# Kernel tuning notes

Hardware: AMD Instinct MI355X
Metric: run time of the kernel (lower is better)

## Reference

```python
import jax, jax.numpy as jnp
import numpy as np

EPS = 1e-5  # nn.BatchNorm2d default eps


def _cbs(x, w, g, b, m, v):
    # Conv(k=1, bias=False) + BatchNorm2d(inference) + SiLU
    y = jnp.einsum('bchw,oc->bohw', x, w)
    s = (g * jax.lax.rsqrt(v + EPS))[None, :, None, None]
    y = (y - m[None, :, None, None]) * s + b[None, :, None, None]
    return y * jax.nn.sigmoid(y)


def setup_inputs():
    key = jax.random.key(0)
    B, D, H, W = 1, 256, 80, 80
    C = D // 2
    ks = jax.random.split(key, 20)
    r = lambda i, shape, sc=1.0: jax.random.normal(ks[i], shape, dtype=jnp.float32) * sc
    oC, oD = jnp.ones((C,), jnp.float32), jnp.ones((D,), jnp.float32)
    zC, zD = jnp.zeros((C,), jnp.float32), jnp.zeros((D,), jnp.float32)
    return {
        'x': r(0, (B, D, H, W)),
        'w1': r(1, (C, D), 0.05), 'g1': oC, 'b1': zC, 'm1': zC, 'v1': oC,
        'w2': r(2, (D, C), 0.05), 'g2': oD, 'b2': zD, 'm2': zD, 'v2': oD,
        'w3': r(3, (D, C), 0.05), 'g3': oD, 'b3': zD, 'm3': zD, 'v3': oD,
        'wq': r(4, (C, C), 0.05), 'bq': r(5, (C,), 0.01),
        'wk': r(6, (C, C), 0.05), 'bk': r(7, (C,), 0.01),
        'wv': r(8, (C, C), 0.05), 'bv': r(9, (C,), 0.01),
        'wp': r(10, (C, C), 0.05), 'bp': r(11, (C,), 0.01),
        'rel_h': r(12, (1, C, H, 1)), 'rel_w': r(13, (1, C, 1, W)),
        'ef_h': r(14, (1, C, H, 1)), 'ef_w': r(15, (1, C, 1, W)),
    }


def reference(x, w1, g1, b1, m1, v1, w2, g2, b2, m2, v2, w3, g3, b3, m3, v3,
              wq, bq, wk, bk, wv, bv, wp, bp, rel_h, rel_w, ef_h, ef_w):
    x1 = _cbs(x, w1, g1, b1, m1, v1)            # [B, C, H, W]
    B, C, H, W = x1.shape
    HW = H * W
    proj = lambda w, b: (jnp.einsum('bchw,oc->bohw', x1, w)
                         + b[None, :, None, None]).reshape(B, C, HW)
    q = proj(wq, bq)
    k = proj(wk, bk)
    v = proj(wv, bv)
    p = proj(wp, bp)
    # content-content + content-position attention branch
    cp = (rel_h + rel_w).reshape(C, HW)          # [C, HW]
    cc = jnp.einsum('bci,bcj->bij', q, k)        # [B, HW, HW]
    cpos = jnp.einsum('ci,bcj->bij', cp, q)      # [B, HW, HW]
    attn = jax.nn.softmax(cc + cpos, axis=-1)
    # out1[b,c,i] = sum_j v[b,c,j] * attn[b,i,j]  (bmm(v, attn^T))
    out1 = jnp.einsum('bcj,bij->bci', v, attn).reshape(B, C, H, W)
    # extra positional branch (valid because B == 1)
    ef = (ef_h + ef_w).reshape(B, C, HW)         # [1, C, HW]
    ce = jnp.einsum('bci,bcj->bij', p, ef)       # [B, HW, HW]
    eng = jax.nn.softmax(ce, axis=-1)
    out2 = jnp.einsum('bcj,bij->bci', ef, eng).reshape(B, C, H, W)
    return x + _cbs(out1, w2, g2, b2, m2, v2) + _cbs(out2, w3, g3, b3, m3, v3)
```

## Files before the change

kernel.cpp:

```cpp
#include <hip/hip_runtime.h>


typedef unsigned short u16;
typedef __attribute__((ext_vector_type(8))) short bf16x8;
typedef __attribute__((ext_vector_type(4))) float f32x4;
typedef __attribute__((ext_vector_type(4))) unsigned int u32x4;

#define HW 6400
#define BN_EPS 1e-5f

__device__ __forceinline__ u16 f2b(float f) {
  unsigned u = __float_as_uint(f);
  u += 0x7fffu + ((u >> 16) & 1u);
  return (u16)(u >> 16);
}
__device__ __forceinline__ unsigned pack2(float a, float b) {
  return (unsigned)f2b(a) | ((unsigned)f2b(b) << 16);
}
__device__ __forceinline__ f32x4 MFMA(bf16x8 a, bf16x8 b, f32x4 c) {
  return __builtin_amdgcn_mfma_f32_16x16x32_bf16(a, b, c, 0, 0, 0);
}
__device__ __forceinline__ float silu_f(float y) {
  return y / (1.0f + __expf(-y));
}
__device__ __forceinline__ bf16x8 pack8(f32x4 lo, f32x4 hi, float sc) {
  union { bf16x8 v; uint4 u; } r;
  r.u.x = pack2(lo[0] * sc, lo[1] * sc);
  r.u.y = pack2(lo[2] * sc, lo[3] * sc);
  r.u.z = pack2(hi[0] * sc, hi[1] * sc);
  r.u.w = pack2(hi[2] * sc, hi[3] * sc);
  return r.v;
}
__device__ __forceinline__ void unpack8(bf16x8 v, f32x4& lo, f32x4& hi) {
  union { bf16x8 v; unsigned short e[8]; } u; u.v = v;
#pragma unroll
  for (int k = 0; k < 4; ++k) {
    lo[k] = __uint_as_float((unsigned)u.e[k] << 16);
    hi[k] = __uint_as_float((unsigned)u.e[k + 4] << 16);
  }
}
__device__ __forceinline__ void gload_lds16(const u16* src, u16* dst) {
  __builtin_amdgcn_global_load_lds(
      (const __attribute__((address_space(1))) void*)src,
      (__attribute__((address_space(3))) void*)dst, 16, 0, 0);
}

__global__ void prep_all(
    const float* __restrict__ rel_h, const float* __restrict__ rel_w,
    const float* __restrict__ ef_h, const float* __restrict__ ef_w,
    const float* __restrict__ w1, const float* __restrict__ g1, const float* __restrict__ b1,
    const float* __restrict__ m1, const float* __restrict__ v1,
    const float* __restrict__ w2, const float* __restrict__ g2, const float* __restrict__ b2,
    const float* __restrict__ m2, const float* __restrict__ v2,
    const float* __restrict__ w3, const float* __restrict__ g3, const float* __restrict__ b3,
    const float* __restrict__ m3, const float* __restrict__ v3,
    const float* __restrict__ wq, const float* __restrict__ bq,
    const float* __restrict__ wk, const float* __restrict__ bk,
    const float* __restrict__ wv, const float* __restrict__ bv,
    const float* __restrict__ wp, const float* __restrict__ bp,
    u16* __restrict__ LT,
    u16* __restrict__ w1b, float* __restrict__ b1e,
    u16* __restrict__ Wcat, float* __restrict__ bcat,
    u16* __restrict__ w2b, float* __restrict__ b2e,
    u16* __restrict__ w3b, float* __restrict__ b3e,
    u16* __restrict__ efhT, u16* __restrict__ efwT,
    u16* __restrict__ efhB, u16* __restrict__ efwB,
    float* __restrict__ lbuf)
{
  const int b = blockIdx.x;
  const int t = threadIdx.x;
  if (b < 80) {
    const int h = b;
    const int c0 = (t & 63) * 2;
    const float rh0 = rel_h[c0 * 80 + h], rh1 = rel_h[(c0 + 1) * 80 + h];
    for (int wcol = (t >> 6); wcol < 80; wcol += 4) {
      const int i = h * 80 + wcol;
      float rw0 = rel_w[c0 * 80 + wcol], rw1 = rel_w[(c0 + 1) * 80 + wcol];
      *(unsigned*)&LT[(size_t)i * 256 + 128 + c0] = pack2(rh0 + rw0, rh1 + rw1);
    }
  } else if (b < 144) {
    const int tid = (b - 80) * 256 + t;
    const int stride = 64 * 256;
    for (int idx = tid; idx < 128 * 256; idx += stride) {
      int o = idx >> 8;
      float s = g1[o] * rsqrtf(v1[o] + BN_EPS);
      w1b[idx] = f2b(w1[idx] * s);
    }
    for (int idx = tid; idx < 128; idx += stride) {
      float s = g1[idx] * rsqrtf(v1[idx] + BN_EPS);
      b1e[idx] = b1[idx] - m1[idx] * s;
    }
    for (int idx = tid; idx < 4 * 128 * 128; idx += stride) {
      int which = idx >> 14, r = idx & 16383;
      const float* src = which == 0 ? wq : which == 1 ? wk : which == 2 ? wv : wp;
      Wcat[idx] = f2b(src[r]);
    }
    for (int idx = tid; idx < 512; idx += stride) {
      int which = idx >> 7, r = idx & 127;
      const float* src = which == 0 ? bq : which == 1 ? bk : which == 2 ? bv : bp;
      bcat[idx] = src[r];
    }
    for (int idx = tid; idx < 256 * 128; idx += stride) {
      int o = idx >> 7;
      float s2 = g2[o] * rsqrtf(v2[o] + BN_EPS);
      w2b[idx] = f2b(w2[idx] * s2);
      float s3 = g3[o] * rsqrtf(v3[o] + BN_EPS);
      w3b[idx] = f2b(w3[idx] * s3);
    }
    for (int idx = tid; idx < 256; idx += stride) {
      float s2 = g2[idx] * rsqrtf(v2[idx] + BN_EPS);
      b2e[idx] = b2[idx] - m2[idx] * s2;
      float s3 = g3[idx] * rsqrtf(v3[idx] + BN_EPS);
      b3e[idx] = b3[idx] - m3[idx] * s3;
    }
    for (int idx = tid; idx < 80 * 128; idx += stride) {
      int hj = idx >> 7, c = idx & 127;
      efhT[idx] = f2b(ef_h[c * 80 + hj]);
      efwT[idx] = f2b(ef_w[c * 80 + hj]);
    }
    for (int idx = tid; idx < 128 * 96; idx += stride) {
      int c = idx / 96, hj = idx % 96;
      efhB[idx] = hj < 80 ? f2b(ef_h[c * 80 + hj]) : (u16)0;
      efwB[idx] = hj < 80 ? f2b(ef_w[c * 80 + hj]) : (u16)0;
    }
  } else {
    const int tid = (b - 144) * 256 + t;
    const int stride = 32 * 256;
    for (int idx = tid; idx < HW / 4; idx += stride)
      ((f32x4*)lbuf)[idx] = (f32x4){0.f, 0.f, 0.f, 0.f};
  }
}

__global__ __launch_bounds__(256) void front_k(
    const float* __restrict__ x,
    const u16* __restrict__ w1b, const float* __restrict__ b1e,
    const u16* __restrict__ Wcat, const float* __restrict__ bcat,
    u16* __restrict__ LT, u16* __restrict__ RT, u16* __restrict__ Vv,
    u16* __restrict__ pT)
{
  __shared__ __align__(16) float xs[16][260];
  __shared__ __align__(16) u16 tr[16][136];
  const int t = threadIdx.x, lane = t & 63, w = t >> 6, jl = lane & 15, q = lane >> 4;
  const bool partA = blockIdx.x < 400;
  const int ib = partA ? blockIdx.x : blockIdx.x - 400;
  const int i0 = ib * 16;

#pragma unroll
  for (int pp = 0; pp < 4; ++pp) {
    const int p = w * 4 + pp;
    const int ch = p * 16 + (lane >> 2);
    const int ii = (lane & 3) * 4;
    f32x4 v = *(const f32x4*)(x + (size_t)ch * HW + i0 + ii);
    xs[ii][ch] = v[0]; xs[ii + 1][ch] = v[1];
    xs[ii + 2][ch] = v[2]; xs[ii + 3][ch] = v[3];
  }
  __syncthreads();

  bf16x8 afr[8];
#pragma unroll
  for (int ks = 0; ks < 8; ++ks) {
    f32x4 va = *(const f32x4*)&xs[jl][ks * 32 + q * 8];
    f32x4 vb = *(const f32x4*)&xs[jl][ks * 32 + q * 8 + 4];
    afr[ks] = pack8(va, vb, 1.0f);
  }
  f32x4 acc[2];
#pragma unroll
  for (int nn = 0; nn < 2; ++nn) acc[nn] = (f32x4){0.f, 0.f, 0.f, 0.f};
#pragma unroll
  for (int ks = 0; ks < 8; ++ks)
#pragma unroll
    for (int nn = 0; nn < 2; ++nn) {
      const int nf = w * 2 + nn;
      bf16x8 b = *(const bf16x8*)(w1b + (size_t)(nf * 16 + jl) * 256 + ks * 32 + q * 8);
      acc[nn] = MFMA(afr[ks], b, acc[nn]);
    }
#pragma unroll
  for (int nn = 0; nn < 2; ++nn) {
    const int c = (w * 2 + nn) * 16 + jl;
    const float bias = b1e[c];
#pragma unroll
    for (int r = 0; r < 4; ++r)
      tr[q * 4 + r][c] = f2b(silu_f(acc[nn][r] + bias));
  }
  __syncthreads();
  bf16x8 xa[4];
#pragma unroll
  for (int ks = 0; ks < 4; ++ks)
    xa[ks] = *(const bf16x8*)&tr[jl][ks * 32 + q * 8];

  for (int ncl = 0; ncl < 2; ++ncl) {
    const int nc = (partA ? 0 : 2) + ncl;
    f32x4 a2[2];
#pragma unroll
    for (int nn = 0; nn < 2; ++nn) a2[nn] = (f32x4){0.f, 0.f, 0.f, 0.f};
#pragma unroll
    for (int ks = 0; ks < 4; ++ks)
#pragma unroll
      for (int nn = 0; nn < 2; ++nn) {
        const int nf = w * 2 + nn;
        bf16x8 b = *(const bf16x8*)(Wcat + (size_t)(nc * 128 + nf * 16 + jl) * 128 + ks * 32 + q * 8);
        a2[nn] = MFMA(xa[ks], b, a2[nn]);
      }
    if (nc == 2) {
#pragma unroll
      for (int nn = 0; nn < 2; ++nn) {
        const int c = (w * 2 + nn) * 16 + jl;
        const float bias = bcat[256 + c];
        uint2 pk;
        pk.x = pack2(a2[nn][0] + bias, a2[nn][1] + bias);
        pk.y = pack2(a2[nn][2] + bias, a2[nn][3] + bias);
        *(uint2*)(Vv + (size_t)c * HW + i0 + q * 4) = pk;
      }
    } else {
      __syncthreads();
#pragma unroll
      for (int nn = 0; nn < 2; ++nn) {
        const int c = (w * 2 + nn) * 16 + jl;
        const float bias = bcat[nc * 128 + c];
#pragma unroll
        for (int r = 0; r < 4; ++r)
          tr[q * 4 + r][c] = f2b(a2[nn][r] + bias);
      }
      __syncthreads();
#pragma unroll
      for (int rr = 0; rr < 4; ++rr) {
        const int r = w * 4 + rr;
        unsigned val = *(const unsigned*)&tr[r][lane * 2];
        const size_t row = (size_t)(i0 + r);
        if (nc == 0) {
          *(unsigned*)(LT + row * 256 + lane * 2) = val;
          *(unsigned*)(RT + row * 256 + 128 + lane * 2) = val;
        } else if (nc == 1) {
          *(unsigned*)(RT + row * 256 + lane * 2) = val;
        } else {
          *(unsigned*)(pT + row * 128 + lane * 2) = val;
        }
      }
    }
  }
}

__global__ __launch_bounds__(512, 2) void fused_attn(
    const u16* __restrict__ LT,
    const u16* __restrict__ RT,
    const u16* __restrict__ Vv,
    u16* __restrict__ Opart,
    float* __restrict__ lv)
{
  __shared__ __align__(1024) u16 Rs[2][128 * 128];
  __shared__ __align__(1024) u16 Ts[2][64 * 128];
  const int t = threadIdx.x, lane = t & 63, w = t >> 6, jl = lane & 15, q = lane >> 4;
  const int bid = blockIdx.x;
  const int jp = bid / 50, it = bid % 50;
  const int wi = w & 1, wj = w >> 1;
  const int i0w = it * 128 + wi * 64;
  u16* Tw = Ts[wi];

  bf16x8 afr[4][8];
#pragma unroll
  for (int mt = 0; mt < 4; ++mt)
#pragma unroll
    for (int l = 0; l < 8; ++l)
      afr[mt][l] = *(const bf16x8*)(LT + (size_t)(i0w + mt * 16 + jl) * 256 + l * 32 + q * 8);

  f32x4 o[4][2];
#pragma unroll
  for (int mt = 0; mt < 4; ++mt)
#pragma unroll
    for (int cf = 0; cf < 2; ++cf) o[mt][cf] = (f32x4){0.f, 0.f, 0.f, 0.f};
  float lacc[4] = {0.f, 0.f, 0.f, 0.f};

  auto stage_half = [&](int jj, int b) {
#pragma unroll
    for (int cl = 0; cl < 4; ++cl) {
      const int cc = w * 4 + cl;
      const int jr = cc * 4 + (lane >> 4);
      const int cp = lane & 15;
      const int ch = (cp & ~7) | ((cp ^ jr) & 7);
      gload_lds16(RT + (size_t)(jj + jr) * 256 + b * 128 + ch * 8,
                  Rs[b] + (cc << 9));
    }
  };

  stage_half(jp * 1280, 0);
  stage_half(jp * 1280, 1);

  for (int stp = 0; stp < 10; ++stp) {
    const int jj = jp * 1280 + stp * 128;

    f32x4 s[2][4];
#pragma unroll
    for (int nf = 0; nf < 2; ++nf)
#pragma unroll
      for (int mt = 0; mt < 4; ++mt) s[nf][mt] = (f32x4){0.f, 0.f, 0.f, 0.f};

    __syncthreads();

#pragma unroll
    for (int h = 0; h < 2; ++h)
#pragma unroll
      for (int nf = 0; nf < 2; ++nf) {
        const int row = wj * 32 + nf * 16 + jl;
#pragma unroll
        for (int l = 0; l < 4; ++l) {
          const int ch = (l * 4 + q) ^ (jl & 7);
          bf16x8 b = *(const bf16x8*)(Rs[h] + row * 128 + ch * 8);
          s[nf][0] = MFMA(b, afr[0][h * 4 + l], s[nf][0]);
          s[nf][1] = MFMA(b, afr[1][h * 4 + l], s[nf][1]);
          s[nf][2] = MFMA(b, afr[2][h * 4 + l], s[nf][2]);
          s[nf][3] = MFMA(b, afr[3][h * 4 + l], s[nf][3]);
        }
      }
    __syncthreads();
    if (stp < 9) stage_half(jj + 128, 0);

#pragma unroll
    for (int nf = 0; nf < 2; ++nf)
#pragma unroll
      for (int mt = 0; mt < 4; ++mt)
#pragma unroll
        for (int r = 0; r < 4; ++r) {
          float p = __expf(s[nf][mt][r]);
          s[nf][mt][r] = p;
          lacc[mt] += p;
        }

#pragma unroll
    for (int mt = 0; mt < 4; ++mt)
#pragma unroll
      for (int nf = 0; nf < 2; ++nf) {
        const int row = mt * 16 + jl;
        const int cs = (wj * 8 + nf * 4 + q) ^ ((jl & 7) << 2);
        uint2 pk;
        pk.x = pack2(s[nf][mt][0], s[nf][mt][1]);
        pk.y = pack2(s[nf][mt][2], s[nf][mt][3]);
        *(uint2*)(Tw + row * 128 + cs * 4) = pk;
      }
    __syncthreads();
    if (stp < 9) stage_half(jj + 128, 1);

#pragma unroll
    for (int ks2 = 0; ks2 < 4; ++ks2) {
      bf16x8 bv0 = *(const bf16x8*)(Vv + (size_t)(wj * 32 + jl) * HW + jj + ks2 * 32 + q * 8);
      bf16x8 bv1 = *(const bf16x8*)(Vv + (size_t)(wj * 32 + 16 + jl) * HW + jj + ks2 * 32 + q * 8);
      const int cb = (ks2 * 8 + q * 2) ^ ((jl & 7) << 2);
#pragma unroll
      for (int mt = 0; mt < 4; ++mt) {
        bf16x8 pa = *(const bf16x8*)(Tw + (mt * 16 + jl) * 128 + cb * 4);
        o[mt][0] = MFMA(pa, bv0, o[mt][0]);
        o[mt][1] = MFMA(pa, bv1, o[mt][1]);
      }
    }
  }

#pragma unroll
  for (int mt = 0; mt < 4; ++mt) {
    float rsum = lacc[mt];
    rsum += __shfl_xor(rsum, 16);
    rsum += __shfl_xor(rsum, 32);
    if (lane < 16)
      atomicAdd(&lv[i0w + mt * 16 + jl], rsum);
  }
#pragma unroll
  for (int mt = 0; mt < 4; ++mt) {
    const int ib = i0w + mt * 16 + q * 4;
#pragma unroll
    for (int cf = 0; cf < 2; ++cf) {
      const int c = wj * 32 + cf * 16 + jl;
#pragma unroll
      for (int r = 0; r < 4; ++r)
        Opart[((size_t)(ib + r) * 5 + jp) * 128 + c] = f2b(o[mt][cf][r]);
    }
  }
}

__global__ __launch_bounds__(512, 2) void final2(
    const u16* __restrict__ pT,
    const u16* __restrict__ efhT, const u16* __restrict__ efwT,
    const u16* __restrict__ efhB, const u16* __restrict__ efwB,
    const u16* __restrict__ Opart,
    const float* __restrict__ lv,
    const u16* __restrict__ w2b, const float* __restrict__ b2e,
    const u16* __restrict__ w3b, const float* __restrict__ b3e,
    const float* __restrict__ x, float* __restrict__ outp)
{
  __shared__ __align__(16) u16 eAs[32][104];
  __shared__ __align__(16) u16 eBs[32][104];
  __shared__ float sAL[32], sBL[32];
  __shared__ __align__(16) u16 T2[32][136];
  const int t = threadIdx.x, lane = t & 63, w = t >> 6, jl = lane & 15, q = lane >> 4;
  const int rg = w & 1, ncl = w >> 1;
  const int i0 = blockIdx.x * 32;
  const int rowA = i0 + rg * 16 + jl;
  const int iloc = rg * 16 + jl;

  if (ncl == 0) {
    bf16x8 pfr[4];
#pragma unroll
    for (int l = 0; l < 4; ++l)
      pfr[l] = *(const bf16x8*)(pT + (size_t)rowA * 128 + l * 32 + q * 8);
    f32x4 sa[5], sb[5];
#pragma unroll
    for (int nf = 0; nf < 5; ++nf) {
      sa[nf] = (f32x4){0.f, 0.f, 0.f, 0.f};
      sb[nf] = (f32x4){0.f, 0.f, 0.f, 0.f};
    }
#pragma unroll
    for (int nf = 0; nf < 5; ++nf) {
      const int row = nf * 16 + jl;
#pragma unroll
      for (int l = 0; l < 4; ++l) {
        bf16x8 eh = *(const bf16x8*)(efhT + (size_t)row * 128 + l * 32 + q * 8);
        bf16x8 ew = *(const bf16x8*)(efwT + (size_t)row * 128 + l * 32 + q * 8);
        sa[nf] = MFMA(eh, pfr[l], sa[nf]);
        sb[nf] = MFMA(ew, pfr[l], sb[nf]);
      }
    }
    float ra = 0.f, rb = 0.f;
#pragma unroll
    for (int nf = 0; nf < 5; ++nf) {
      float ea[4], eb[4];
#pragma unroll
      for (int r = 0; r < 4; ++r) {
        ea[r] = __expf(sa[nf][r]); ra += ea[r];
        eb[r] = __expf(sb[nf][r]); rb += eb[r];
      }
      uint2 pa, pb;
      pa.x = pack2(ea[0], ea[1]); pa.y = pack2(ea[2], ea[3]);
      pb.x = pack2(eb[0], eb[1]); pb.y = pack2(eb[2], eb[3]);
      *(uint2*)&eAs[iloc][nf * 16 + q * 4] = pa;
      *(uint2*)&eBs[iloc][nf * 16 + q * 4] = pb;
    }
    *(uint2*)&eAs[iloc][80 + q * 4] = (uint2){0u, 0u};
    *(uint2*)&eBs[iloc][80 + q * 4] = (uint2){0u, 0u};
    ra += __shfl_xor(ra, 16); ra += __shfl_xor(ra, 32);
    rb += __shfl_xor(rb, 16); rb += __shfl_xor(rb, 32);
    if (lane < 16) { sAL[iloc] = ra; sBL[iloc] = rb; }
  }
  __syncthreads();

  if (ncl == 1) {
    bf16x8 fa[3], fb[3];
#pragma unroll
    for (int l = 0; l < 3; ++l) {
      fa[l] = *(const bf16x8*)&eAs[iloc][l * 32 + q * 8];
      fb[l] = *(const bf16x8*)&eBs[iloc][l * 32 + q * 8];
    }
    f32x4 oU[8], oW[8];
#pragma unroll
    for (int nf = 0; nf < 8; ++nf) {
      oU[nf] = (f32x4){0.f, 0.f, 0.f, 0.f};
      oW[nf] = (f32x4){0.f, 0.f, 0.f, 0.f};
    }
#pragma unroll
    for (int l = 0; l < 3; ++l)
#pragma unroll
      for (int nf = 0; nf < 8; ++nf) {
        bf16x8 bh = *(const bf16x8*)(efhB + (size_t)(nf * 16 + jl) * 96 + l * 32 + q * 8);
        bf16x8 bw = *(const bf16x8*)(efwB + (size_t)(nf * 16 + jl) * 96 + l * 32 + q * 8);
        oU[nf] = MFMA(fa[l], bh, oU[nf]);
        oW[nf] = MFMA(fb[l], bw, oW[nf]);
      }
    float ia[4], iw[4];
#pragma unroll
    for (int r = 0; r < 4; ++r) {
      ia[r] = 1.0f / sAL[rg * 16 + q * 4 + r];
      iw[r] = 1.0f / sBL[rg * 16 + q * 4 + r];
    }
#pragma unroll
    for (int nf = 0; nf < 8; ++nf)
#pragma unroll
      for (int r = 0; r < 4; ++r)
        T2[rg * 16 + q * 4 + r][nf * 16 + jl] =
            f2b(oU[nf][r] * ia[r] + oW[nf][r] * iw[r]);
  }
  __syncthreads();

  const float inv1 = 1.0f / lv[rowA];
  const u16* OrBase = Opart + (size_t)rowA * 5 * 128;
  f32x4 a1[4], a2[4];
#pragma unroll
  for (int nf = 0; nf < 4; ++nf) {
    a1[nf] = (f32x4){0.f, 0.f, 0.f, 0.f};
    a2[nf] = (f32x4){0.f, 0.f, 0.f, 0.f};
  }
#pragma unroll
  for (int ks = 0; ks < 4; ++ks) {
    f32x4 s1a = (f32x4){0.f, 0.f, 0.f, 0.f};
    f32x4 s1b = (f32x4){0.f, 0.f, 0.f, 0.f};
#pragma unroll
    for (int p = 0; p < 5; ++p) {
      bf16x8 pv = *(const bf16x8*)(OrBase + p * 128 + ks * 32 + q * 8);
      f32x4 lo, hi;
      unpack8(pv, lo, hi);
      s1a += lo;
      s1b += hi;
    }
    bf16x8 fa1 = pack8(s1a, s1b, inv1);
    bf16x8 fa2 = *(const bf16x8*)&T2[rg * 16 + jl][ks * 32 + q * 8];
#pragma unroll
    for (int nf = 0; nf < 4; ++nf) {
      const int d = ncl * 64 + nf * 16 + jl;
      bf16x8 b2f = *(const bf16x8*)(w2b + (size_t)d * 128 + ks * 32 + q * 8);
      bf16x8 b3f = *(const bf16x8*)(w3b + (size_t)d * 128 + ks * 32 + q * 8);
      a1[nf] = MFMA(fa1, b2f, a1[nf]);
      a2[nf] = MFMA(fa2, b3f, a2[nf]);
    }
  }
#pragma unroll
  for (int nf = 0; nf < 4; ++nf) {
    const int d = ncl * 64 + nf * 16 + jl;
    const float bb2 = b2e[d], bb3 = b3e[d];
    const size_t base = (size_t)d * HW + i0 + rg * 16 + q * 4;
    f32x4 xv = *(const f32x4*)(x + base);
    f32x4 rv;
#pragma unroll
    for (int r = 0; r < 4; ++r)
      rv[r] = xv[r] + silu_f(a1[nf][r] + bb2) + silu_f(a2[nf][r] + bb3);
    *(f32x4*)(outp + base) = rv;
  }
}

extern "C" void kernel_launch(void* const* d_in, const int* in_sizes, int n_in,
                              void* d_out, int out_size, void* d_ws, size_t ws_size,
                              hipStream_t stream)
{
  (void)in_sizes; (void)n_in; (void)out_size; (void)ws_size;
  const float* x   = (const float*)d_in[0];
  const float* w1  = (const float*)d_in[1];
  const float* g1  = (const float*)d_in[2];
  const float* b1  = (const float*)d_in[3];
  const float* m1  = (const float*)d_in[4];
  const float* v1  = (const float*)d_in[5];
  const float* w2  = (const float*)d_in[6];
  const float* g2  = (const float*)d_in[7];
  const float* b2  = (const float*)d_in[8];
  const float* m2  = (const float*)d_in[9];
  const float* v2  = (const float*)d_in[10];
  const float* w3  = (const float*)d_in[11];
  const float* g3  = (const float*)d_in[12];
  const float* b3  = (const float*)d_in[13];
  const float* m3  = (const float*)d_in[14];
  const float* v3  = (const float*)d_in[15];
  const float* wq  = (const float*)d_in[16];
  const float* bq  = (const float*)d_in[17];
  const float* wk  = (const float*)d_in[18];
  const float* bk  = (const float*)d_in[19];
  const float* wv  = (const float*)d_in[20];
  const float* bv  = (const float*)d_in[21];
  const float* wp  = (const float*)d_in[22];
  const float* bp  = (const float*)d_in[23];
  const float* rel_h = (const float*)d_in[24];
  const float* rel_w = (const float*)d_in[25];
  const float* ef_h  = (const float*)d_in[26];
  const float* ef_w  = (const float*)d_in[27];
  float* outp = (float*)d_out;

  char* ws = (char*)d_ws;
  size_t off = 0;
  auto alloc = [&](size_t bytes) -> void* {
    void* p = ws + off;
    off += (bytes + 511) & ~(size_t)511;
    return p;
  };
  u16* LT    = (u16*)alloc((size_t)HW * 256 * 2);
  u16* RT    = (u16*)alloc((size_t)HW * 256 * 2);
  u16* pT    = (u16*)alloc((size_t)HW * 128 * 2);
  u16* Vv    = (u16*)alloc((size_t)HW * 128 * 2);
  u16* Opart = (u16*)alloc((size_t)HW * 5 * 128 * 2);
  float* lbuf  = (float*)alloc((size_t)HW * 4);
  u16* w1b   = (u16*)alloc(128 * 256 * 2);
  float* b1e = (float*)alloc(128 * 4);
  u16* Wcat  = (u16*)alloc(512 * 128 * 2);
  float* bcat = (float*)alloc(512 * 4);
  u16* w2b   = (u16*)alloc(256 * 128 * 2);
  float* b2e = (float*)alloc(256 * 4);
  u16* w3b   = (u16*)alloc(256 * 128 * 2);
  float* b3e = (float*)alloc(256 * 4);
  u16* efhT  = (u16*)alloc(80 * 128 * 2);
  u16* efwT  = (u16*)alloc(80 * 128 * 2);
  u16* efhB  = (u16*)alloc(128 * 96 * 2);
  u16* efwB  = (u16*)alloc(128 * 96 * 2);

  prep_all<<<176, 256, 0, stream>>>(rel_h, rel_w, ef_h, ef_w,
                                    w1, g1, b1, m1, v1, w2, g2, b2, m2, v2,
                                    w3, g3, b3, m3, v3, wq, bq, wk, bk, wv, bv, wp, bp,
                                    LT, w1b, b1e, Wcat, bcat, w2b, b2e, w3b, b3e,
                                    efhT, efwT, efhB, efwB, lbuf);
  front_k<<<800, 256, 0, stream>>>(x, w1b, b1e, Wcat, bcat, LT, RT, Vv, pT);
  fused_attn<<<250, 512, 0, stream>>>(LT, RT, Vv, Opart, lbuf);
  final2<<<dim3(200), 512, 0, stream>>>(pT, efhT, efwT, efhB, efwB,
                                        Opart, lbuf, w2b, b2e, w3b, b3e,
                                        x, outp);
}
```

Baseline: 215.4 us.

## Issue full next-tile prefetch at once and restructure final2 to per-wave redundant work

In the attention kernel, both halves of the next R tile are now staged right after the score barrier, rather than the second half waiting until after the probability store. In final2, each block handles 16 rows with 256 threads. Every wave computes the positional-branch softmax for those rows redundantly into its own LDS slice, then syncs with a wave-local lgkmcnt wait instead of block barriers. This removes idle waves and block-wide barriers in final2, at the cost of four times the redundant positional-branch work. The earlier prefetch may also race with reads of Rs[1] in the same step if any wave is still reading it.

```diff
diff --git a/kernel.cpp b/kernel.cpp
--- a/kernel.cpp
+++ b/kernel.cpp
@@ -43,6 +43,11 @@
   __builtin_amdgcn_global_load_lds(
       (const __attribute__((address_space(1))) void*)src,
       (__attribute__((address_space(3))) void*)dst, 16, 0, 0);
+}
+__device__ __forceinline__ void lds_fence() {
+  __builtin_amdgcn_sched_barrier(0);
+  asm volatile("s_waitcnt lgkmcnt(0)" ::: "memory");
+  __builtin_amdgcn_sched_barrier(0);
 }
 
 __global__ void prep_all(
@@ -270,9 +275,10 @@
     for (int cf = 0; cf < 2; ++cf) o[mt][cf] = (f32x4){0.f, 0.f, 0.f, 0.f};
   float lacc[4] = {0.f, 0.f, 0.f, 0.f};
 
-  auto stage_half = [&](int jj, int b) {
-#pragma unroll
-    for (int cl = 0; cl < 4; ++cl) {
+  auto stage = [&](int jj) {
+#pragma unroll
+    for (int k = 0; k < 8; ++k) {
+      const int b = k >> 2, cl = k & 3;
       const int cc = w * 4 + cl;
       const int jr = cc * 4 + (lane >> 4);
       const int cp = lane & 15;
@@ -282,8 +288,7 @@
     }
   };
 
-  stage_half(jp * 1280, 0);
-  stage_half(jp * 1280, 1);
+  stage(jp * 1280);
 
   for (int stp = 0; stp < 10; ++stp) {
     const int jj = jp * 1280 + stp * 128;
@@ -312,7 +317,7 @@
         }
       }
     __syncthreads();
-    if (stp < 9) stage_half(jj + 128, 0);
+    if (stp < 9) stage(jj + 128);
 
 #pragma unroll
     for (int nf = 0; nf < 2; ++nf)
@@ -337,7 +342,6 @@
         *(uint2*)(Tw + row * 128 + cs * 4) = pk;
       }
     __syncthreads();
-    if (stp < 9) stage_half(jj + 128, 1);
 
 #pragma unroll
     for (int ks2 = 0; ks2 < 4; ++ks2) {
@@ -374,7 +378,7 @@
   }
 }
 
-__global__ __launch_bounds__(512, 2) void final2(
+__global__ __launch_bounds__(256) void final2(
     const u16* __restrict__ pT,
     const u16* __restrict__ efhT, const u16* __restrict__ efwT,
     const u16* __restrict__ efhB, const u16* __restrict__ efwB,
@@ -384,17 +388,15 @@
     const u16* __restrict__ w3b, const float* __restrict__ b3e,
     const float* __restrict__ x, float* __restrict__ outp)
 {
-  __shared__ __align__(16) u16 eAs[32][104];
-  __shared__ __align__(16) u16 eBs[32][104];
-  __shared__ float sAL[32], sBL[32];
-  __shared__ __align__(16) u16 T2[32][136];
+  __shared__ __align__(16) u16 eAs[4][16][104];
+  __shared__ __align__(16) u16 eBs[4][16][104];
+  __shared__ __align__(16) u16 T2[4][16][136];
+  __shared__ float sAL[4][16], sBL[4][16];
   const int t = threadIdx.x, lane = t & 63, w = t >> 6, jl = lane & 15, q = lane >> 4;
-  const int rg = w & 1, ncl = w >> 1;
-  const int i0 = blockIdx.x * 32;
-  const int rowA = i0 + rg * 16 + jl;
-  const int iloc = rg * 16 + jl;
-
-  if (ncl == 0) {
+  const int i0 = blockIdx.x * 16;
+  const int rowA = i0 + jl;
+
+  {
     bf16x8 pfr[4];
 #pragma unroll
     for (int l = 0; l < 4; ++l)
@@ -428,23 +430,23 @@
       uint2 pa, pb;
       pa.x = pack2(ea[0], ea[1]); pa.y = pack2(ea[2], ea[3]);
       pb.x = pack2(eb[0], eb[1]); pb.y = pack2(eb[2], eb[3]);
-      *(uint2*)&eAs[iloc][nf * 16 + q * 4] = pa;
-      *(uint2*)&eBs[iloc][nf * 16 + q * 4] = pb;
-    }
-    *(uint2*)&eAs[iloc][80 + q * 4] = (uint2){0u, 0u};
-    *(uint2*)&eBs[iloc][80 + q * 4] = (uint2){0u, 0u};
+      *(uint2*)&eAs[w][jl][nf * 16 + q * 4] = pa;
+      *(uint2*)&eBs[w][jl][nf * 16 + q * 4] = pb;
+    }
+    *(uint2*)&eAs[w][jl][80 + q * 4] = (uint2){0u, 0u};
+    *(uint2*)&eBs[w][jl][80 + q * 4] = (uint2){0u, 0u};
     ra += __shfl_xor(ra, 16); ra += __shfl_xor(ra, 32);
     rb += __shfl_xor(rb, 16); rb += __shfl_xor(rb, 32);
-    if (lane < 16) { sAL[iloc] = ra; sBL[iloc] = rb; }
-  }
-  __syncthreads();
-
-  if (ncl == 1) {
+    if (lane < 16) { sAL[w][jl] = ra; sBL[w][jl] = rb; }
+  }
+  lds_fence();
+
+  {
     bf16x8 fa[3], fb[3];
 #pragma unroll
     for (int l = 0; l < 3; ++l) {
-      fa[l] = *(const bf16x8*)&eAs[iloc][l * 32 + q * 8];
-      fb[l] = *(const bf16x8*)&eBs[iloc][l * 32 + q * 8];
+      fa[l] = *(const bf16x8*)&eAs[w][jl][l * 32 + q * 8];
+      fb[l] = *(const bf16x8*)&eBs[w][jl][l * 32 + q * 8];
     }
     f32x4 oU[8], oW[8];
 #pragma unroll
@@ -464,17 +466,17 @@
     float ia[4], iw[4];
 #pragma unroll
     for (int r = 0; r < 4; ++r) {
-      ia[r] = 1.0f / sAL[rg * 16 + q * 4 + r];
-      iw[r] = 1.0f / sBL[rg * 16 + q * 4 + r];
+      ia[r] = 1.0f / sAL[w][q * 4 + r];
+      iw[r] = 1.0f / sBL[w][q * 4 + r];
     }
 #pragma unroll
     for (int nf = 0; nf < 8; ++nf)
 #pragma unroll
       for (int r = 0; r < 4; ++r)
-        T2[rg * 16 + q * 4 + r][nf * 16 + jl] =
+        T2[w][q * 4 + r][nf * 16 + jl] =
             f2b(oU[nf][r] * ia[r] + oW[nf][r] * iw[r]);
   }
-  __syncthreads();
+  lds_fence();
 
   const float inv1 = 1.0f / lv[rowA];
   const u16* OrBase = Opart + (size_t)rowA * 5 * 128;
@@ -497,10 +499,10 @@
       s1b += hi;
     }
     bf16x8 fa1 = pack8(s1a, s1b, inv1);
-    bf16x8 fa2 = *(const bf16x8*)&T2[rg * 16 + jl][ks * 32 + q * 8];
+    bf16x8 fa2 = *(const bf16x8*)&T2[w][jl][ks * 32 + q * 8];
 #pragma unroll
     for (int nf = 0; nf < 4; ++nf) {
-      const int d = ncl * 64 + nf * 16 + jl;
+      const int d = w * 64 + nf * 16 + jl;
       bf16x8 b2f = *(const bf16x8*)(w2b + (size_t)d * 128 + ks * 32 + q * 8);
       bf16x8 b3f = *(const bf16x8*)(w3b + (size_t)d * 128 + ks * 32 + q * 8);
       a1[nf] = MFMA(fa1, b2f, a1[nf]);
@@ -509,9 +511,9 @@
   }
 #pragma unroll
   for (int nf = 0; nf < 4; ++nf) {
-    const int d = ncl * 64 + nf * 16 + jl;
+    const int d = w * 64 + nf * 16 + jl;
     const float bb2 = b2e[d], bb3 = b3e[d];
-    const size_t base = (size_t)d * HW + i0 + rg * 16 + q * 4;
+    const size_t base = (size_t)d * HW + i0 + q * 4;
     f32x4 xv = *(const f32x4*)(x + base);
     f32x4 rv;
 #pragma unroll
@@ -589,7 +591,7 @@
                                     efhT, efwT, efhB, efwB, lbuf);
   front_k<<<800, 256, 0, stream>>>(x, w1b, b1e, Wcat, bcat, LT, RT, Vv, pT);
   fused_attn<<<250, 512, 0, stream>>>(LT, RT, Vv, Opart, lbuf);
-  final2<<<dim3(200), 512, 0, stream>>>(pT, efhT, efwT, efhB, efwB,
-                                        Opart, lbuf, w2b, b2e, w3b, b3e,
-                                        x, outp);
-}
+  final2<<<400, 256, 0, stream>>>(pT, efhT, efwT, efhB, efwB,
+                                  Opart, lbuf, w2b, b2e, w3b, b3e,
+                                  x, outp);
+}
```

After: 220.2 us. 1.02x slower.
